# Performance work log

Hardware: AMD Instinct MI355X
Metric: run time of the kernel (lower is better)

## Reference

```python
import jax, jax.numpy as jnp
import numpy as np

NEG_INF = -1.0e9  # matches the source's close_to_negative_inf


def setup_inputs() -> dict:
    key = jax.random.key(0)
    k1, k2, k3, k4 = jax.random.split(key, 4)
    B, S, H, Dh = 2, 2048, 16, 64
    d_model = H * Dh
    return {
        "pre_q": jax.random.normal(k1, (B, S, H, Dh), dtype=jnp.float32),
        "pre_v": jax.random.normal(k2, (B, S, H, Dh), dtype=jnp.float32),
        "pre_k": jax.random.normal(k3, (B, S, H, Dh), dtype=jnp.float32),
        "output_weights": jax.random.normal(k4, (d_model, d_model), dtype=jnp.float32) * (1.0 / np.sqrt(d_model)),
        "out_seq_len": S,
        "d_model": d_model,
    }


def reference(pre_q, pre_v, pre_k, output_weights, out_seq_len, d_model):
    B, S, H, Dh = pre_q.shape
    # (B, H, S, Dh)
    q = jnp.transpose(pre_q, (0, 2, 1, 3))
    k = jnp.transpose(pre_k, (0, 2, 1, 3))
    v = jnp.transpose(pre_v, (0, 2, 1, 3))
    scale = 1.0 / jnp.sqrt(jnp.float32(Dh))
    # scaled QK^T: (B, H, Sq, Sk)
    scores = jnp.einsum("bhqd,bhkd->bhqk", q, k) * scale
    # source masking: multiply by lower triangle, add -1e9 on upper triangle
    tril = jnp.tril(jnp.ones((S, S), dtype=scores.dtype))
    masked = tril * scores + NEG_INF * (1.0 - tril)
    attn = jax.nn.softmax(masked, axis=-1)
    heads = jnp.einsum("bhqk,bhkd->bhqd", attn, v)  # (B, H, S, Dh)
    merged = jnp.transpose(heads, (0, 2, 1, 3)).reshape(B, S, H * Dh)
    out = jnp.einsum("bsd,de->bse", merged, output_weights)
    return out.reshape(-1, out_seq_len, d_model)
```

## Files before the change

### kernel.cpp

```cpp
#include <hip/hip_runtime.h>
#include <stdint.h>

#define S_LEN 2048
#define NH 16
#define DH 64
#define DM 1024

typedef __attribute__((ext_vector_type(8))) short short8;
typedef __attribute__((ext_vector_type(4))) float f32x4;

__device__ __forceinline__ unsigned short f2bf(float f) {
  union { float f; uint32_t u; } c; c.f = f;
  uint32_t u = c.u;
  return (unsigned short)((u + 0x7FFFu + ((u >> 16) & 1u)) >> 16);
}

__device__ __forceinline__ uint32_t pk_bf16(float lo, float hi) {
  uint32_t r;
  asm("v_cvt_pk_bf16_f32 %0, %1, %2" : "=v"(r) : "v"(lo), "v"(hi));
  return r;
}

__device__ __forceinline__ void g2l16(const void* g, void* l) {
  __builtin_amdgcn_global_load_lds(
      (const __attribute__((address_space(1))) uint32_t*)g,
      (__attribute__((address_space(3))) uint32_t*)l, 16, 0, 0);
}

#define PL32(a, b) asm("v_permlane32_swap_b32 %0, %1" : "+v"(a), "+v"(b))
#define PL16(a, b) asm("v_permlane16_swap_b32 %0, %1" : "+v"(a), "+v"(b))

__global__ __launch_bounds__(256) void prep_kernel(const float* __restrict__ K,
                                                   const float* __restrict__ V,
                                                   const float* __restrict__ W,
                                                   unsigned short* __restrict__ Kb,
                                                   unsigned short* __restrict__ Vt,
                                                   unsigned short* __restrict__ Wt) {
  __shared__ __align__(16) unsigned short tile[64 * 72];
  const int tid = threadIdx.x;
  const int blk = blockIdx.x;

  if (blk >= 1024) {
    const int wb = blk - 1024;
    const int e0 = (wb & 15) << 6;
    const int d0 = (wb >> 4) << 6;
#pragma unroll
    for (int i = 0; i < 4; ++i) {
      int idx = tid + i * 256;
      int d = idx >> 4;
      int ec = (idx & 15) << 2;
      float4 w = *(const float4*)(W + (size_t)(d0 + d) * DM + e0 + ec);
      tile[(ec + 0) * 72 + d] = f2bf(w.x);
      tile[(ec + 1) * 72 + d] = f2bf(w.y);
      tile[(ec + 2) * 72 + d] = f2bf(w.z);
      tile[(ec + 3) * 72 + d] = f2bf(w.w);
    }
    __syncthreads();
#pragma unroll
    for (int i = 0; i < 2; ++i) {
      int idx = tid + i * 256;
      int e = idx >> 3;
      int g = idx & 7;
      uint4 v = *(const uint4*)&tile[e * 72 + (g << 3)];
      *(uint4*)(Wt + (size_t)(e0 + e) * DM + d0 + ((g ^ (e & 7)) << 3)) = v;
    }
    return;
  }

  const int st = blk & 31;
  const int bh = blk >> 5;
  const int b = bh >> 4;
  const int h = bh & 15;
  const int s0 = st << 6;
  const size_t ibase = (size_t)b * (S_LEN * DM) + (size_t)h * DH;
  const size_t kbase = (size_t)bh * (S_LEN * DH);
  const size_t vbase = (size_t)bh * (DH * S_LEN);

#pragma unroll
  for (int i = 0; i < 4; ++i) {
    int idx = tid + i * 256;
    int s = idx >> 4;
    int d4 = (idx & 15) << 2;
    int g = d4 >> 3, rem = d4 & 7;
    float4 kv = *(const float4*)(K + ibase + (size_t)(s0 + s) * DM + d4);
    uint2 u;
    u.x = pk_bf16(kv.x, kv.y);
    u.y = pk_bf16(kv.z, kv.w);
    *(uint2*)(Kb + kbase + (size_t)(s0 + s) * DH + ((g ^ (s & 7)) << 3) + rem) = u;
  }
#pragma unroll
  for (int i = 0; i < 4; ++i) {
    int idx = tid + i * 256;
    int s = idx >> 4;
    int d4 = (idx & 15) << 2;
    float4 vv = *(const float4*)(V + ibase + (size_t)(s0 + s) * DM + d4);
    tile[(d4 + 0) * 72 + s] = f2bf(vv.x);
    tile[(d4 + 1) * 72 + s] = f2bf(vv.y);
    tile[(d4 + 2) * 72 + s] = f2bf(vv.z);
    tile[(d4 + 3) * 72 + s] = f2bf(vv.w);
  }
  __syncthreads();
#pragma unroll
  for (int i = 0; i < 2; ++i) {
    int idx = tid + i * 256;
    int d = idx >> 3;
    int g = idx & 7;
    uint4 u = *(const uint4*)&tile[d * 72 + (g << 3)];
    *(uint4*)(Vt + vbase + (size_t)d * S_LEN + s0 + ((g ^ (d & 7)) << 3)) = u;
  }
}

__global__ __launch_bounds__(256) void attn_kernel(const float* __restrict__ Q,
                                                   const unsigned short* __restrict__ Kb,
                                                   const unsigned short* __restrict__ Vt,
                                                   unsigned short* __restrict__ merged) {
  __shared__ __align__(16) unsigned short kbuf[3][64 * 64];
  __shared__ __align__(16) unsigned short vbuf[3][64 * 64];

  const int tid = threadIdx.x;
  const int wave = tid >> 6;
  const int lane = tid & 63;
  const int t = lane & 15;
  const int qd = lane >> 4;
  const int tx = t & 7;

  const int bid = blockIdx.x;
  const int qt = 31 - (bid >> 5);
  const int bh = bid & 31;
  const int h = bh & 15;
  const int b = bh >> 4;

  const int q0 = qt << 6;
  const int row0 = q0 + (wave << 4);
  const size_t qbase = (size_t)b * (S_LEN * DM) + (size_t)h * DH;
  const unsigned short* kg = Kb + (size_t)bh * (S_LEN * DH);
  const unsigned short* vg = Vt + (size_t)bh * (DH * S_LEN);

  short8 qfrag[2];
  {
    const float SC = 0.125f * 1.4426950408889634f;
    const float* qp = Q + qbase + (size_t)(row0 + t) * DM + (qd << 3);
#pragma unroll
    for (int kk = 0; kk < 2; ++kk) {
      float4 f0 = *(const float4*)(qp + kk * 32);
      float4 f1 = *(const float4*)(qp + kk * 32 + 4);
      union { short8 s; uint32_t u[4]; } qq;
      qq.u[0] = pk_bf16(f0.x * SC, f0.y * SC);
      qq.u[1] = pk_bf16(f0.z * SC, f0.w * SC);
      qq.u[2] = pk_bf16(f1.x * SC, f1.y * SC);
      qq.u[3] = pk_bf16(f1.z * SC, f1.w * SC);
      qfrag[kk] = qq.s;
    }
  }

  const int c1 = wave * 512;
  const int c2 = (wave + 4) * 512;
  const int l8 = lane * 8;
  auto stage = [&](int bsel, int kt0) {
    g2l16(kg + (size_t)kt0 * DH + c1 + l8, &kbuf[bsel][c1]);
    g2l16(kg + (size_t)kt0 * DH + c2 + l8, &kbuf[bsel][c2]);
    int o1 = c1 + l8, o2 = c2 + l8;
    g2l16(vg + (size_t)(o1 >> 6) * S_LEN + kt0 + (o1 & 63), &vbuf[bsel][c1]);
    g2l16(vg + (size_t)(o2 >> 6) * S_LEN + kt0 + (o2 & 63), &vbuf[bsel][c2]);
  };

  const f32x4 fzero = {0.f, 0.f, 0.f, 0.f};
  float lsum = 0.f;
  f32x4 o_acc[4];
#pragma unroll
  for (int nb = 0; nb < 4; ++nb) o_acc[nb] = fzero;

  const int ntiles = qt + 1;
  stage(0, 0);
  if (ntiles > 1) stage(1, 64);
  int b0 = 0, b1 = 1, b2 = 2;

  for (int tile = 0; tile < ntiles; ++tile) {
    if (tile + 1 < ntiles)
      asm volatile("s_waitcnt vmcnt(4)" ::: "memory");
    else
      asm volatile("s_waitcnt vmcnt(0)" ::: "memory");
    __builtin_amdgcn_s_barrier();
    asm volatile("" ::: "memory");
    if (tile + 2 < ntiles) stage(b2, (tile + 2) << 6);

    const unsigned short* kl = kbuf[b0];
    const unsigned short* vl = vbuf[b0];

    f32x4 sc[4];
#pragma unroll
    for (int cb = 0; cb < 4; ++cb) {
      const int row = cb * 16 + t;
      short8 a0 = *(const short8*)&kl[row * 64 + ((qd ^ tx) << 3)];
      short8 a1 = *(const short8*)&kl[row * 64 + (((4 | qd) ^ tx) << 3)];
      f32x4 a = fzero;
      a = __builtin_amdgcn_mfma_f32_16x16x32_bf16(a0, qfrag[0], a, 0, 0, 0);
      a = __builtin_amdgcn_mfma_f32_16x16x32_bf16(a1, qfrag[1], a, 0, 0, 0);
      sc[cb] = a;
    }

    if (tile == ntiles - 1) {
#pragma unroll
      for (int cb = 0; cb < 4; ++cb)
#pragma unroll
        for (int r = 0; r < 4; ++r)
          if ((tile << 6) + cb * 16 + qd * 4 + r > row0 + t) sc[cb][r] = -INFINITY;
    }

#pragma unroll
    for (int cb = 0; cb < 4; ++cb)
#pragma unroll
      for (int r = 0; r < 4; ++r)
        sc[cb][r] = __builtin_amdgcn_exp2f(sc[cb][r]);
    lsum += ((sc[0][0] + sc[0][1]) + (sc[0][2] + sc[0][3])) +
            ((sc[1][0] + sc[1][1]) + (sc[1][2] + sc[1][3])) +
            ((sc[2][0] + sc[2][1]) + (sc[2][2] + sc[2][3])) +
            ((sc[3][0] + sc[3][1]) + (sc[3][2] + sc[3][3]));

    uint32_t p00 = pk_bf16(sc[0][0], sc[0][1]);
    uint32_t p01 = pk_bf16(sc[0][2], sc[0][3]);
    uint32_t p10 = pk_bf16(sc[1][0], sc[1][1]);
    uint32_t p11 = pk_bf16(sc[1][2], sc[1][3]);
    uint32_t p20 = pk_bf16(sc[2][0], sc[2][1]);
    uint32_t p21 = pk_bf16(sc[2][2], sc[2][3]);
    uint32_t p30 = pk_bf16(sc[3][0], sc[3][1]);
    uint32_t p31 = pk_bf16(sc[3][2], sc[3][3]);
    PL32(p00, p10); PL32(p01, p11);
    PL16(p00, p10); PL16(p01, p11);
    PL32(p20, p30); PL32(p21, p31);
    PL16(p20, p30); PL16(p21, p31);
    union { short8 s; uint32_t u[4]; } pa0, pa1;
    pa0.u[0] = p00; pa0.u[1] = p01; pa0.u[2] = p10; pa0.u[3] = p11;
    pa1.u[0] = p20; pa1.u[1] = p21; pa1.u[2] = p30; pa1.u[3] = p31;

#pragma unroll
    for (int nb = 0; nb < 4; ++nb) {
      short8 v0 = *(const short8*)&vl[(nb * 16 + t) * 64 + ((qd ^ tx) << 3)];
      o_acc[nb] = __builtin_amdgcn_mfma_f32_16x16x32_bf16(v0, pa0.s, o_acc[nb], 0, 0, 0);
      short8 v1 = *(const short8*)&vl[(nb * 16 + t) * 64 + (((4 | qd) ^ tx) << 3)];
      o_acc[nb] = __builtin_amdgcn_mfma_f32_16x16x32_bf16(v1, pa1.s, o_acc[nb], 0, 0, 0);
    }

    int tb = b0; b0 = b1; b1 = b2; b2 = tb;
  }

  lsum += __shfl_xor(lsum, 16);
  lsum += __shfl_xor(lsum, 32);
  const float invl = __builtin_amdgcn_rcpf(lsum);

  uint32_t e00 = pk_bf16(o_acc[0][0] * invl, o_acc[0][1] * invl);
  uint32_t e01 = pk_bf16(o_acc[0][2] * invl, o_acc[0][3] * invl);
  uint32_t e10 = pk_bf16(o_acc[1][0] * invl, o_acc[1][1] * invl);
  uint32_t e11 = pk_bf16(o_acc[1][2] * invl, o_acc[1][3] * invl);
  uint32_t e20 = pk_bf16(o_acc[2][0] * invl, o_acc[2][1] * invl);
  uint32_t e21 = pk_bf16(o_acc[2][2] * invl, o_acc[2][3] * invl);
  uint32_t e30 = pk_bf16(o_acc[3][0] * invl, o_acc[3][1] * invl);
  uint32_t e31 = pk_bf16(o_acc[3][2] * invl, o_acc[3][3] * invl);
  PL32(e00, e20); PL32(e10, e30);
  PL16(e00, e10); PL16(e20, e30);
  PL32(e01, e21); PL32(e11, e31);
  PL16(e01, e11); PL16(e21, e31);
  union { uint4 v; uint32_t u[4]; } u0, u1;
  u0.u[0] = e00; u0.u[1] = e01; u0.u[2] = e10; u0.u[3] = e11;
  u1.u[0] = e20; u1.u[1] = e21; u1.u[2] = e30; u1.u[3] = e31;
  unsigned short* mp = merged + (size_t)(b * S_LEN + row0 + t) * DM + h * DH;
  *(uint4*)(mp + (((2 * qd) ^ tx) << 3)) = u0.v;
  *(uint4*)(mp + (((2 * qd + 1) ^ tx) << 3)) = u1.v;
}

__global__ __launch_bounds__(256) void gemm_kernel(const unsigned short* __restrict__ A,
                                                   const unsigned short* __restrict__ Bt,
                                                   float* __restrict__ C) {
  __shared__ __align__(16) unsigned short abuf[2][128 * 64];
  __shared__ __align__(16) unsigned short bbuf[2][128 * 64];
  const int tid = threadIdx.x;
  const int wave = tid >> 6;
  const int lane = tid & 63;
  const int t = lane & 15;
  const int qd = lane >> 4;
  const int tx = t & 7;
  const int wm = wave >> 1;
  const int wn = wave & 1;
  const int n0 = blockIdx.x << 7;
  const int m0 = blockIdx.y << 7;

  const int rin = lane >> 3;
  const int cin = (lane & 7) << 3;
  auto stage = [&](int bsel, int kt) {
#pragma unroll
    for (int i = 0; i < 4; ++i) {
      int c = wave * 4 + i;
      int row = c * 8 + rin;
      g2l16(A + (size_t)(m0 + row) * DM + kt + cin, &abuf[bsel][c * 512]);
      g2l16(Bt + (size_t)(n0 + row) * DM + kt + cin, &bbuf[bsel][c * 512]);
    }
  };

  const f32x4 fzero = {0.f, 0.f, 0.f, 0.f};
  f32x4 acc[4][4];
#pragma unroll
  for (int mi = 0; mi < 4; ++mi)
#pragma unroll
    for (int nb = 0; nb < 4; ++nb) acc[mi][nb] = fzero;

  stage(0, 0);
  int cur = 0;

  for (int kt = 0; kt < DM; kt += 64) {
    asm volatile("s_waitcnt vmcnt(0)" ::: "memory");
    __builtin_amdgcn_s_barrier();
    asm volatile("" ::: "memory");
    if (kt + 64 < DM) stage(cur ^ 1, kt + 64);
    const unsigned short* al = abuf[cur];
    const unsigned short* bl = bbuf[cur];
#pragma unroll
    for (int kk = 0; kk < 2; ++kk) {
      const int sw = ((kk * 4 + qd) ^ tx) << 3;
      short8 af[4], bf[4];
#pragma unroll
      for (int mi = 0; mi < 4; ++mi)
        af[mi] = *(const short8*)&al[(wm * 64 + mi * 16 + t) * 64 + sw];
#pragma unroll
      for (int nb = 0; nb < 4; ++nb)
        bf[nb] = *(const short8*)&bl[(wn * 64 + nb * 16 + t) * 64 + sw];
#pragma unroll
      for (int mi = 0; mi < 4; ++mi)
#pragma unroll
        for (int nb = 0; nb < 4; ++nb)
          acc[mi][nb] = __builtin_amdgcn_mfma_f32_16x16x32_bf16(af[mi], bf[nb], acc[mi][nb], 0, 0, 0);
    }
    cur ^= 1;
  }
#pragma unroll
  for (int mi = 0; mi < 4; ++mi)
#pragma unroll
    for (int nb = 0; nb < 4; ++nb)
#pragma unroll
      for (int r = 0; r < 4; ++r)
        C[(size_t)(m0 + wm * 64 + mi * 16 + qd * 4 + r) * DM + n0 + wn * 64 + nb * 16 + t] =
            acc[mi][nb][r];
}

extern "C" void kernel_launch(void* const* d_in, const int* in_sizes, int n_in,
                              void* d_out, int out_size, void* d_ws, size_t ws_size,
                              hipStream_t stream) {
  const float* pre_q = (const float*)d_in[0];
  const float* pre_v = (const float*)d_in[1];
  const float* pre_k = (const float*)d_in[2];
  const float* W     = (const float*)d_in[3];
  float* out = (float*)d_out;

  unsigned short* Wt = (unsigned short*)d_ws;
  unsigned short* merged = Wt + (size_t)DM * DM;
  unsigned short* Kb = merged + (size_t)4096 * DM;
  unsigned short* Vt = Kb + (size_t)32 * S_LEN * DH;

  prep_kernel<<<dim3(1280), 256, 0, stream>>>(pre_k, pre_v, W, Kb, Vt, Wt);
  attn_kernel<<<dim3(1024), 256, 0, stream>>>(pre_q, Kb, Vt, merged);
  gemm_kernel<<<dim3(8, 32), 256, 0, stream>>>(merged, Wt, out);
}
```

Before: 152.5 us.

## Process 128-row query tiles per block to reuse staged K/V across two row groups

```diff
diff --git a/kernel.cpp b/kernel.cpp
--- a/kernel.cpp
+++ b/kernel.cpp
@@ -125,31 +125,37 @@
   const int tx = t & 7;
 
   const int bid = blockIdx.x;
-  const int qt = 31 - (bid >> 5);
   const int bh = bid & 31;
+  const int r8 = (bid >> 5) & 7;
+  const int cc = bid >> 8;
+  const int qt = cc ? r8 : (15 - r8);
+
   const int h = bh & 15;
   const int b = bh >> 4;
 
-  const int q0 = qt << 6;
-  const int row0 = q0 + (wave << 4);
+  const int q0 = qt << 7;
+  const int rw = wave << 5;
   const size_t qbase = (size_t)b * (S_LEN * DM) + (size_t)h * DH;
   const unsigned short* kg = Kb + (size_t)bh * (S_LEN * DH);
   const unsigned short* vg = Vt + (size_t)bh * (DH * S_LEN);
 
-  short8 qfrag[2];
+  short8 qfrag[2][2];
   {
     const float SC = 0.125f * 1.4426950408889634f;
-    const float* qp = Q + qbase + (size_t)(row0 + t) * DM + (qd << 3);
-#pragma unroll
-    for (int kk = 0; kk < 2; ++kk) {
-      float4 f0 = *(const float4*)(qp + kk * 32);
-      float4 f1 = *(const float4*)(qp + kk * 32 + 4);
-      union { short8 s; uint32_t u[4]; } qq;
-      qq.u[0] = pk_bf16(f0.x * SC, f0.y * SC);
-      qq.u[1] = pk_bf16(f0.z * SC, f0.w * SC);
-      qq.u[2] = pk_bf16(f1.x * SC, f1.y * SC);
-      qq.u[3] = pk_bf16(f1.z * SC, f1.w * SC);
-      qfrag[kk] = qq.s;
+#pragma unroll
+    for (int gg = 0; gg < 2; ++gg) {
+      const float* qp = Q + qbase + (size_t)(q0 + rw + gg * 16 + t) * DM + (qd << 3);
+#pragma unroll
+      for (int kk = 0; kk < 2; ++kk) {
+        float4 f0 = *(const float4*)(qp + kk * 32);
+        float4 f1 = *(const float4*)(qp + kk * 32 + 4);
+        union { short8 s; uint32_t u[4]; } qq;
+        qq.u[0] = pk_bf16(f0.x * SC, f0.y * SC);
+        qq.u[1] = pk_bf16(f0.z * SC, f0.w * SC);
+        qq.u[2] = pk_bf16(f1.x * SC, f1.y * SC);
+        qq.u[3] = pk_bf16(f1.z * SC, f1.w * SC);
+        qfrag[gg][kk] = qq.s;
+      }
     }
   }
 
@@ -165,14 +171,16 @@
   };
 
   const f32x4 fzero = {0.f, 0.f, 0.f, 0.f};
-  float lsum = 0.f;
-  f32x4 o_acc[4];
-#pragma unroll
-  for (int nb = 0; nb < 4; ++nb) o_acc[nb] = fzero;
-
-  const int ntiles = qt + 1;
+  float lsum[2] = {0.f, 0.f};
+  f32x4 o_acc[2][4];
+#pragma unroll
+  for (int gg = 0; gg < 2; ++gg)
+#pragma unroll
+    for (int nb = 0; nb < 4; ++nb) o_acc[gg][nb] = fzero;
+
+  const int ntiles = (q0 >> 6) + 2;
   stage(0, 0);
-  if (ntiles > 1) stage(1, 64);
+  stage(1, 64);
   int b0 = 0, b1 = 1, b2 = 2;
 
   for (int tile = 0; tile < ntiles; ++tile) {
@@ -184,88 +192,100 @@
     asm volatile("" ::: "memory");
     if (tile + 2 < ntiles) stage(b2, (tile + 2) << 6);
 
-    const unsigned short* kl = kbuf[b0];
-    const unsigned short* vl = vbuf[b0];
-
-    f32x4 sc[4];
-#pragma unroll
-    for (int cb = 0; cb < 4; ++cb) {
-      const int row = cb * 16 + t;
-      short8 a0 = *(const short8*)&kl[row * 64 + ((qd ^ tx) << 3)];
-      short8 a1 = *(const short8*)&kl[row * 64 + (((4 | qd) ^ tx) << 3)];
-      f32x4 a = fzero;
-      a = __builtin_amdgcn_mfma_f32_16x16x32_bf16(a0, qfrag[0], a, 0, 0, 0);
-      a = __builtin_amdgcn_mfma_f32_16x16x32_bf16(a1, qfrag[1], a, 0, 0, 0);
-      sc[cb] = a;
-    }
-
-    if (tile == ntiles - 1) {
-#pragma unroll
-      for (int cb = 0; cb < 4; ++cb)
-#pragma unroll
-        for (int r = 0; r < 4; ++r)
-          if ((tile << 6) + cb * 16 + qd * 4 + r > row0 + t) sc[cb][r] = -INFINITY;
-    }
-
-#pragma unroll
-    for (int cb = 0; cb < 4; ++cb)
-#pragma unroll
-      for (int r = 0; r < 4; ++r)
-        sc[cb][r] = __builtin_amdgcn_exp2f(sc[cb][r]);
-    lsum += ((sc[0][0] + sc[0][1]) + (sc[0][2] + sc[0][3])) +
-            ((sc[1][0] + sc[1][1]) + (sc[1][2] + sc[1][3])) +
-            ((sc[2][0] + sc[2][1]) + (sc[2][2] + sc[2][3])) +
-            ((sc[3][0] + sc[3][1]) + (sc[3][2] + sc[3][3]));
-
-    uint32_t p00 = pk_bf16(sc[0][0], sc[0][1]);
-    uint32_t p01 = pk_bf16(sc[0][2], sc[0][3]);
-    uint32_t p10 = pk_bf16(sc[1][0], sc[1][1]);
-    uint32_t p11 = pk_bf16(sc[1][2], sc[1][3]);
-    uint32_t p20 = pk_bf16(sc[2][0], sc[2][1]);
-    uint32_t p21 = pk_bf16(sc[2][2], sc[2][3]);
-    uint32_t p30 = pk_bf16(sc[3][0], sc[3][1]);
-    uint32_t p31 = pk_bf16(sc[3][2], sc[3][3]);
-    PL32(p00, p10); PL32(p01, p11);
-    PL16(p00, p10); PL16(p01, p11);
-    PL32(p20, p30); PL32(p21, p31);
-    PL16(p20, p30); PL16(p21, p31);
-    union { short8 s; uint32_t u[4]; } pa0, pa1;
-    pa0.u[0] = p00; pa0.u[1] = p01; pa0.u[2] = p10; pa0.u[3] = p11;
-    pa1.u[0] = p20; pa1.u[1] = p21; pa1.u[2] = p30; pa1.u[3] = p31;
-
-#pragma unroll
-    for (int nb = 0; nb < 4; ++nb) {
-      short8 v0 = *(const short8*)&vl[(nb * 16 + t) * 64 + ((qd ^ tx) << 3)];
-      o_acc[nb] = __builtin_amdgcn_mfma_f32_16x16x32_bf16(v0, pa0.s, o_acc[nb], 0, 0, 0);
-      short8 v1 = *(const short8*)&vl[(nb * 16 + t) * 64 + (((4 | qd) ^ tx) << 3)];
-      o_acc[nb] = __builtin_amdgcn_mfma_f32_16x16x32_bf16(v1, pa1.s, o_acc[nb], 0, 0, 0);
+    if (!(tile == ntiles - 1 && wave < 2)) {
+      const unsigned short* kl = kbuf[b0];
+      const unsigned short* vl = vbuf[b0];
+      const int dtile = tile - (ntiles - 2);
+
+#pragma unroll
+      for (int gg = 0; gg < 2; ++gg) {
+        f32x4 sc[4];
+#pragma unroll
+        for (int cb = 0; cb < 4; ++cb) {
+          const int row = cb * 16 + t;
+          short8 a0 = *(const short8*)&kl[row * 64 + ((qd ^ tx) << 3)];
+          short8 a1 = *(const short8*)&kl[row * 64 + (((4 | qd) ^ tx) << 3)];
+          f32x4 a = fzero;
+          a = __builtin_amdgcn_mfma_f32_16x16x32_bf16(a0, qfrag[gg][0], a, 0, 0, 0);
+          a = __builtin_amdgcn_mfma_f32_16x16x32_bf16(a1, qfrag[gg][1], a, 0, 0, 0);
+          sc[cb] = a;
+        }
+
+        if (dtile >= 0) {
+          const int rowloc = rw + gg * 16 + t;
+#pragma unroll
+          for (int cb = 0; cb < 4; ++cb)
+#pragma unroll
+            for (int r2 = 0; r2 < 4; ++r2)
+              if ((dtile << 6) + cb * 16 + qd * 4 + r2 > rowloc) sc[cb][r2] = -INFINITY;
+        }
+
+#pragma unroll
+        for (int cb = 0; cb < 4; ++cb)
+#pragma unroll
+          for (int r2 = 0; r2 < 4; ++r2)
+            sc[cb][r2] = __builtin_amdgcn_exp2f(sc[cb][r2]);
+        lsum[gg] += ((sc[0][0] + sc[0][1]) + (sc[0][2] + sc[0][3])) +
+                    ((sc[1][0] + sc[1][1]) + (sc[1][2] + sc[1][3])) +
+                    ((sc[2][0] + sc[2][1]) + (sc[2][2] + sc[2][3])) +
+                    ((sc[3][0] + sc[3][1]) + (sc[3][2] + sc[3][3]));
+
+        uint32_t p00 = pk_bf16(sc[0][0], sc[0][1]);
+        uint32_t p01 = pk_bf16(sc[0][2], sc[0][3]);
+        uint32_t p10 = pk_bf16(sc[1][0], sc[1][1]);
+        uint32_t p11 = pk_bf16(sc[1][2], sc[1][3]);
+        uint32_t p20 = pk_bf16(sc[2][0], sc[2][1]);
+        uint32_t p21 = pk_bf16(sc[2][2], sc[2][3]);
+        uint32_t p30 = pk_bf16(sc[3][0], sc[3][1]);
+        uint32_t p31 = pk_bf16(sc[3][2], sc[3][3]);
+        PL32(p00, p10); PL32(p01, p11);
+        PL16(p00, p10); PL16(p01, p11);
+        PL32(p20, p30); PL32(p21, p31);
+        PL16(p20, p30); PL16(p21, p31);
+        union { short8 s; uint32_t u[4]; } pa0, pa1;
+        pa0.u[0] = p00; pa0.u[1] = p01; pa0.u[2] = p10; pa0.u[3] = p11;
+        pa1.u[0] = p20; pa1.u[1] = p21; pa1.u[2] = p30; pa1.u[3] = p31;
+
+#pragma unroll
+        for (int nb = 0; nb < 4; ++nb) {
+          short8 v0 = *(const short8*)&vl[(nb * 16 + t) * 64 + ((qd ^ tx) << 3)];
+          o_acc[gg][nb] = __builtin_amdgcn_mfma_f32_16x16x32_bf16(v0, pa0.s, o_acc[gg][nb], 0, 0, 0);
+          short8 v1 = *(const short8*)&vl[(nb * 16 + t) * 64 + (((4 | qd) ^ tx) << 3)];
+          o_acc[gg][nb] = __builtin_amdgcn_mfma_f32_16x16x32_bf16(v1, pa1.s, o_acc[gg][nb], 0, 0, 0);
+        }
+      }
     }
 
     int tb = b0; b0 = b1; b1 = b2; b2 = tb;
   }
 
-  lsum += __shfl_xor(lsum, 16);
-  lsum += __shfl_xor(lsum, 32);
-  const float invl = __builtin_amdgcn_rcpf(lsum);
-
-  uint32_t e00 = pk_bf16(o_acc[0][0] * invl, o_acc[0][1] * invl);
-  uint32_t e01 = pk_bf16(o_acc[0][2] * invl, o_acc[0][3] * invl);
-  uint32_t e10 = pk_bf16(o_acc[1][0] * invl, o_acc[1][1] * invl);
-  uint32_t e11 = pk_bf16(o_acc[1][2] * invl, o_acc[1][3] * invl);
-  uint32_t e20 = pk_bf16(o_acc[2][0] * invl, o_acc[2][1] * invl);
-  uint32_t e21 = pk_bf16(o_acc[2][2] * invl, o_acc[2][3] * invl);
-  uint32_t e30 = pk_bf16(o_acc[3][0] * invl, o_acc[3][1] * invl);
-  uint32_t e31 = pk_bf16(o_acc[3][2] * invl, o_acc[3][3] * invl);
-  PL32(e00, e20); PL32(e10, e30);
-  PL16(e00, e10); PL16(e20, e30);
-  PL32(e01, e21); PL32(e11, e31);
-  PL16(e01, e11); PL16(e21, e31);
-  union { uint4 v; uint32_t u[4]; } u0, u1;
-  u0.u[0] = e00; u0.u[1] = e01; u0.u[2] = e10; u0.u[3] = e11;
-  u1.u[0] = e20; u1.u[1] = e21; u1.u[2] = e30; u1.u[3] = e31;
-  unsigned short* mp = merged + (size_t)(b * S_LEN + row0 + t) * DM + h * DH;
-  *(uint4*)(mp + (((2 * qd) ^ tx) << 3)) = u0.v;
-  *(uint4*)(mp + (((2 * qd + 1) ^ tx) << 3)) = u1.v;
+#pragma unroll
+  for (int gg = 0; gg < 2; ++gg) {
+    float ls = lsum[gg];
+    ls += __shfl_xor(ls, 16);
+    ls += __shfl_xor(ls, 32);
+    const float invl = __builtin_amdgcn_rcpf(ls);
+
+    uint32_t e00 = pk_bf16(o_acc[gg][0][0] * invl, o_acc[gg][0][1] * invl);
+    uint32_t e01 = pk_bf16(o_acc[gg][0][2] * invl, o_acc[gg][0][3] * invl);
+    uint32_t e10 = pk_bf16(o_acc[gg][1][0] * invl, o_acc[gg][1][1] * invl);
+    uint32_t e11 = pk_bf16(o_acc[gg][1][2] * invl, o_acc[gg][1][3] * invl);
+    uint32_t e20 = pk_bf16(o_acc[gg][2][0] * invl, o_acc[gg][2][1] * invl);
+    uint32_t e21 = pk_bf16(o_acc[gg][2][2] * invl, o_acc[gg][2][3] * invl);
+    uint32_t e30 = pk_bf16(o_acc[gg][3][0] * invl, o_acc[gg][3][1] * invl);
+    uint32_t e31 = pk_bf16(o_acc[gg][3][2] * invl, o_acc[gg][3][3] * invl);
+    PL32(e00, e20); PL32(e10, e30);
+    PL16(e00, e10); PL16(e20, e30);
+    PL32(e01, e21); PL32(e11, e31);
+    PL16(e01, e11); PL16(e21, e31);
+    union { uint4 v; uint32_t u[4]; } u0, u1;
+    u0.u[0] = e00; u0.u[1] = e01; u0.u[2] = e10; u0.u[3] = e11;
+    u1.u[0] = e20; u1.u[1] = e21; u1.u[2] = e30; u1.u[3] = e31;
+    const int srow = q0 + rw + gg * 16 + t;
+    unsigned short* mp = merged + (size_t)(b * S_LEN + srow) * DM + h * DH;
+    *(uint4*)(mp + (((2 * qd) ^ tx) << 3)) = u0.v;
+    *(uint4*)(mp + (((2 * qd + 1) ^ tx) << 3)) = u1.v;
+  }
 }
 
 __global__ __launch_bounds__(256) void gemm_kernel(const unsigned short* __restrict__ A,
@@ -356,6 +376,6 @@
   unsigned short* Vt = Kb + (size_t)32 * S_LEN * DH;
 
   prep_kernel<<<dim3(1280), 256, 0, stream>>>(pre_k, pre_v, W, Kb, Vt, Wt);
-  attn_kernel<<<dim3(1024), 256, 0, stream>>>(pre_q, Kb, Vt, merged);
+  attn_kernel<<<dim3(512), 256, 0, stream>>>(pre_q, Kb, Vt, merged);
   gemm_kernel<<<dim3(8, 32), 256, 0, stream>>>(merged, Wt, out);
 }
```

Measured after the change: 168.1 us. 10.2% more time.
